# Kernel optimization log

Measured on AMD Instinct MI355X. Metric: run time of the kernel, lower is better.

## Reference

```python
import jax, jax.numpy as jnp
import numpy as np

INPUT_DIM = 1024
OUTPUT_DIM = 1024
DOWN = INPUT_DIM // 8  # reduction_factor=8
NUM_TOKENS = 2


def setup_inputs() -> dict:
    key = jax.random.key(0)
    k1, k2, k3, k4, k5 = jax.random.split(key, 5)
    B, Sx, Sy = 32, 2048, 512
    x = jax.random.normal(k1, (B, Sx, INPUT_DIM), dtype=jnp.float32)
    y = jax.random.normal(k2, (B, Sy, INPUT_DIM), dtype=jnp.float32)
    # nn.Parameter(torch.rand(...)) -> uniform [0,1)
    latent_tokens = jax.random.uniform(k3, (NUM_TOKENS, INPUT_DIM), dtype=jnp.float32)
    gate = jnp.zeros((1,), dtype=jnp.float32)
    # Conv1d kernel_size=1, no bias == pointwise matmul; kaiming-uniform-ish init
    lim_d = 1.0 / np.sqrt(INPUT_DIM)
    lim_u = 1.0 / np.sqrt(DOWN)
    W_down = jax.random.uniform(k4, (DOWN, INPUT_DIM), dtype=jnp.float32, minval=-lim_d, maxval=lim_d)
    W_up = jax.random.uniform(k5, (OUTPUT_DIM, DOWN), dtype=jnp.float32, minval=-lim_u, maxval=lim_u)
    return {"x": x, "y": y, "latent_tokens": latent_tokens, "gate": gate,
            "W_down": W_down, "W_up": W_up}


def reference(x, y, latent_tokens, gate, W_down, W_up):
    # tokens attend over y:  [B,T,Sy] softmax over Sy
    att_y2t = jax.nn.softmax(jnp.einsum('td,bsd->bts', latent_tokens, y), axis=-1)
    tokens = latent_tokens[None] + jnp.einsum('bts,bsd->btd', att_y2t, y)  # [B,T,D]
    # x attends over tokens: [B,Sx,T] softmax over T
    att_t2x = jax.nn.softmax(jnp.einsum('bsd,btd->bst', x, tokens), axis=-1)
    x_res = jnp.einsum('bst,btd->bsd', att_t2x, tokens)
    x = x + gate * x_res
    # 1x1 conv bottleneck: down -> ReLU -> up (pointwise matmuls)
    z = jax.nn.relu(jnp.einsum('bsd,ed->bse', x, W_down))
    out = jnp.einsum('bse,oe->bso', z, W_up)
    return out
```

## Files before the change

### kernel.cpp

```cpp
#include <hip/hip_runtime.h>
#include <hip/hip_bf16.h>

#define B_N 32
#define SX 2048
#define SY 512
#define DIM 1024
#define NTOK 2
#define DN 128
#define ODIM 1024
#define BM 64
#define QK 256
#define NQ 4

typedef __bf16 bf16;
typedef __bf16 bf16x8 __attribute__((ext_vector_type(8)));
typedef __bf16 bf16x4 __attribute__((ext_vector_type(4)));
typedef float f32x4 __attribute__((ext_vector_type(4)));

__device__ __forceinline__ f32x4 mfma16(bf16x8 a, bf16x8 b, f32x4 c) {
  return __builtin_amdgcn_mfma_f32_16x16x32_bf16(a, b, c, 0, 0, 0);
}

__global__ __launch_bounds__(256) void prep_kernel(const float* __restrict__ Wd,
                                                   const float* __restrict__ Wu,
                                                   bf16* __restrict__ wdb,
                                                   bf16* __restrict__ wub) {
  int i = blockIdx.x * 256 + threadIdx.x;
  if (i < DN * DIM) {
    wdb[i] = (bf16)Wd[i];
    wub[i] = (bf16)Wu[i];
  }
}

__global__ __launch_bounds__(256) void tokens_kernel(const float* __restrict__ y,
                                                     const float* __restrict__ lat,
                                                     const float* __restrict__ gate,
                                                     float* __restrict__ tokens) {
  if (gate[0] == 0.0f) return;
  __shared__ float s_lat[NTOK][DIM];
  __shared__ float s_sc[NTOK][SY];
  int b = blockIdx.x;
  int tid = threadIdx.x, wave = tid >> 6, lane = tid & 63;
  const float* yb = y + (size_t)b * SY * DIM;
  for (int i = tid; i < NTOK * DIM; i += 256) ((float*)s_lat)[i] = lat[i];
  __syncthreads();
  for (int s = wave * 128; s < wave * 128 + 128; ++s) {
    const float* yr = yb + (size_t)s * DIM;
    float d0 = 0.f, d1 = 0.f;
#pragma unroll
    for (int i = 0; i < 4; ++i) {
      f32x4 v = *(const f32x4*)(yr + lane * 4 + i * 256);
      f32x4 l0 = *(const f32x4*)(&s_lat[0][lane * 4 + i * 256]);
      f32x4 l1 = *(const f32x4*)(&s_lat[1][lane * 4 + i * 256]);
      d0 += v[0] * l0[0] + v[1] * l0[1] + v[2] * l0[2] + v[3] * l0[3];
      d1 += v[0] * l1[0] + v[1] * l1[1] + v[2] * l1[2] + v[3] * l1[3];
    }
#pragma unroll
    for (int off = 32; off > 0; off >>= 1) {
      d0 += __shfl_xor(d0, off);
      d1 += __shfl_xor(d1, off);
    }
    if (lane == 0) { s_sc[0][s] = d0; s_sc[1][s] = d1; }
  }
  __syncthreads();
  if (wave < 2) {
    float m = -3.4e38f;
    for (int s = lane; s < SY; s += 64) m = fmaxf(m, s_sc[wave][s]);
#pragma unroll
    for (int off = 32; off > 0; off >>= 1) m = fmaxf(m, __shfl_xor(m, off));
    float sum = 0.f;
    for (int s = lane; s < SY; s += 64) {
      float e = expf(s_sc[wave][s] - m);
      s_sc[wave][s] = e;
      sum += e;
    }
#pragma unroll
    for (int off = 32; off > 0; off >>= 1) sum += __shfl_xor(sum, off);
    float inv = 1.f / sum;
    for (int s = lane; s < SY; s += 64) s_sc[wave][s] *= inv;
  }
  __syncthreads();
  float a0[4] = {0.f, 0.f, 0.f, 0.f}, a1[4] = {0.f, 0.f, 0.f, 0.f};
  for (int s = 0; s < SY; ++s) {
    float p0 = s_sc[0][s], p1 = s_sc[1][s];
    const float* yr = yb + (size_t)s * DIM;
#pragma unroll
    for (int i = 0; i < 4; ++i) {
      float v = yr[tid + i * 256];
      a0[i] += p0 * v;
      a1[i] += p1 * v;
    }
  }
  float* tb = tokens + (size_t)b * NTOK * DIM;
#pragma unroll
  for (int i = 0; i < 4; ++i) {
    tb[tid + i * 256] = s_lat[0][tid + i * 256] + a0[i];
    tb[DIM + tid + i * 256] = s_lat[1][tid + i * 256] + a1[i];
  }
}

__global__ __launch_bounds__(256) void xprime_kernel(const float* __restrict__ x,
                                                     const float* __restrict__ gate,
                                                     const float* __restrict__ tokens,
                                                     float* __restrict__ xp) {
  float g = gate[0];
  if (g == 0.0f) return;
  __shared__ float s_tok[NTOK][DIM];
  __shared__ float s_c[BM][2];
  int tid = threadIdx.x, w = tid >> 6, lane = tid & 63;
  size_t m0 = (size_t)blockIdx.x * BM;
  int b = (int)(m0 / SX);
  const float* xb = x + m0 * DIM;
  const float* tokb = tokens + (size_t)b * NTOK * DIM;
  for (int i = tid; i < NTOK * DIM; i += 256) ((float*)s_tok)[i] = tokb[i];
  __syncthreads();
  for (int i = 0; i < 16; ++i) {
    int r = w * 16 + i;
    const float* xrow = xb + (size_t)r * DIM;
    float d0 = 0.f, d1 = 0.f;
#pragma unroll
    for (int c = 0; c < 4; ++c) {
      f32x4 v = *(const f32x4*)(xrow + lane * 4 + c * 256);
      f32x4 t0 = *(const f32x4*)(&s_tok[0][lane * 4 + c * 256]);
      f32x4 t1 = *(const f32x4*)(&s_tok[1][lane * 4 + c * 256]);
      d0 += v[0] * t0[0] + v[1] * t0[1] + v[2] * t0[2] + v[3] * t0[3];
      d1 += v[0] * t1[0] + v[1] * t1[1] + v[2] * t1[2] + v[3] * t1[3];
    }
#pragma unroll
    for (int off = 32; off > 0; off >>= 1) {
      d0 += __shfl_xor(d0, off);
      d1 += __shfl_xor(d1, off);
    }
    if (lane == 0) {
      float mm = fmaxf(d0, d1);
      float e0 = expf(d0 - mm), e1 = expf(d1 - mm);
      float inv = g / (e0 + e1);
      s_c[r][0] = e0 * inv;
      s_c[r][1] = e1 * inv;
    }
  }
  __syncthreads();
  float* xpb = xp + m0 * DIM;
  for (int r = w * 16; r < w * 16 + 16; ++r) {
    float c0 = s_c[r][0], c1 = s_c[r][1];
#pragma unroll
    for (int c = 0; c < 4; ++c) {
      f32x4 v = *(const f32x4*)(xb + (size_t)r * DIM + lane * 4 + c * 256);
      f32x4 t0 = *(const f32x4*)(&s_tok[0][lane * 4 + c * 256]);
      f32x4 t1 = *(const f32x4*)(&s_tok[1][lane * 4 + c * 256]);
      f32x4 o;
#pragma unroll
      for (int j = 0; j < 4; ++j) o[j] = v[j] + c0 * t0[j] + c1 * t1[j];
      *(f32x4*)(xpb + (size_t)r * DIM + lane * 4 + c * 256) = o;
    }
  }
}

__global__ __launch_bounds__(512, 4) void main_kernel(const float* __restrict__ x,
                                                      const float* __restrict__ gate,
                                                      const float* __restrict__ xp,
                                                      const bf16* __restrict__ wdb,
                                                      const bf16* __restrict__ wub,
                                                      float* __restrict__ out) {
  __shared__ bf16 xq[2][BM * QK];
  __shared__ bf16 zsm[BM * DN];

  int tid = threadIdx.x, w = tid >> 6, lane = tid & 63;
  int lq = lane >> 4, lr = lane & 15;
  size_t m0 = (size_t)blockIdx.x * BM;
  float g = gate[0];
  const float* xb = ((g != 0.f) ? xp : x) + m0 * DIM;

  int srow = tid >> 5;
  int scolb = (tid & 31) * 16;
  const float* xgp = xb + (size_t)srow * DIM + (tid & 31) * 8;

  f32x4 xs0[4], xs1[4];
  bf16x8 wdr[8];
  f32x4 acc[4] = {};

  const bf16* wdp = wdb + (size_t)(w * 16 + lr) * DIM + lq * 8;

  char* xls = (char*)xq;
  char* zls = (char*)zsm;

  auto XLOAD = [&](int q) {
#pragma unroll
    for (int i = 0; i < 4; ++i) {
      const float* p = xgp + (size_t)i * 16 * DIM + q * QK;
      xs0[i] = *(const f32x4*)p;
      xs1[i] = *(const f32x4*)(p + 4);
    }
  };
  auto WLOAD = [&](int q) {
#pragma unroll
    for (int kc = 0; kc < 8; ++kc)
      wdr[kc] = *(const bf16x8*)(wdp + q * QK + kc * 32);
  };
  auto XWRITE = [&](int buf) {
    char* base = xls + buf * (BM * QK * 2);
#pragma unroll
    for (int i = 0; i < 4; ++i) {
      int row = i * 16 + srow;
      bf16x8 o;
#pragma unroll
      for (int j = 0; j < 4; ++j) {
        o[j] = (bf16)xs0[i][j];
        o[4 + j] = (bf16)xs1[i][j];
      }
      *(bf16x8*)(base + row * (QK * 2) + (scolb ^ ((row & 7) << 4))) = o;
    }
  };
  auto COMP = [&](int buf) {
    const char* base = xls + buf * (BM * QK * 2);
#pragma unroll
    for (int kc = 0; kc < 8; ++kc) {
#pragma unroll
      for (int mt = 0; mt < 4; ++mt) {
        int row = mt * 16 + lr;
        bf16x8 xf = *(const bf16x8*)(base + row * (QK * 2) +
                                     ((kc * 64 + lq * 16) ^ ((row & 7) << 4)));
        acc[mt] = mfma16(wdr[kc], xf, acc[mt]);
      }
    }
  };

  XLOAD(0);
  WLOAD(0);
  XWRITE(0);
  __syncthreads();

#pragma unroll
  for (int q = 0; q < NQ; ++q) {
    if (q + 1 < NQ) XLOAD(q + 1);
    COMP(q & 1);
    if (q + 1 < NQ) WLOAD(q + 1);
    __syncthreads();
    if (q + 1 < NQ) XWRITE((q + 1) & 1);
    __syncthreads();
  }

#pragma unroll
  for (int mt = 0; mt < 4; ++mt) {
    int xr = mt * 16 + lr;
    int dn = w * 16 + lq * 4;
    bf16x4 pk;
#pragma unroll
    for (int r = 0; r < 4; ++r) pk[r] = (bf16)fmaxf(acc[mt][r], 0.f);
    *(bf16x4*)(zls + xr * (DN * 2) + ((dn * 2) ^ ((xr & 7) << 4))) = pk;
  }
  __syncthreads();

  bf16x8 zF[4][4];
#pragma unroll
  for (int mt = 0; mt < 4; ++mt)
#pragma unroll
    for (int kt = 0; kt < 4; ++kt) {
      int xr = mt * 16 + lr;
      zF[kt][mt] = *(const bf16x8*)(zls + xr * (DN * 2) +
                                    (((kt * 32 + lq * 8) * 2) ^ ((xr & 7) << 4)));
    }

  float* ob = out + m0 * ODIM;
#pragma unroll 2
  for (int oc16 = 0; oc16 < 8; ++oc16) {
    int base = w * 128 + oc16 * 16;
    bf16x8 wu[4];
#pragma unroll
    for (int kt = 0; kt < 4; ++kt)
      wu[kt] = *(const bf16x8*)(wub + (size_t)(base + lr) * DN + kt * 32 + lq * 8);
    f32x4 a2[4] = {};
#pragma unroll
    for (int kt = 0; kt < 4; ++kt)
#pragma unroll
      for (int mt = 0; mt < 4; ++mt)
        a2[mt] = mfma16(wu[kt], zF[kt][mt], a2[mt]);
#pragma unroll
    for (int mt = 0; mt < 4; ++mt)
      *(f32x4*)(ob + (size_t)(mt * 16 + lr) * ODIM + base + lq * 4) = a2[mt];
  }
}

extern "C" void kernel_launch(void* const* d_in, const int* in_sizes, int n_in,
                              void* d_out, int out_size, void* d_ws, size_t ws_size,
                              hipStream_t stream) {
  const float* x = (const float*)d_in[0];
  const float* y = (const float*)d_in[1];
  const float* lat = (const float*)d_in[2];
  const float* gate = (const float*)d_in[3];
  const float* Wd = (const float*)d_in[4];
  const float* Wu = (const float*)d_in[5];
  float* out = (float*)d_out;
  char* ws = (char*)d_ws;

  float* tokens = (float*)ws;
  bf16* wdb = (bf16*)(ws + 262144);
  bf16* wub = (bf16*)(ws + 524288);

  prep_kernel<<<(DN * DIM + 255) / 256, 256, 0, stream>>>(Wd, Wu, wdb, wub);
  tokens_kernel<<<B_N, 256, 0, stream>>>(y, lat, gate, tokens);
  xprime_kernel<<<(B_N * SX) / BM, 256, 0, stream>>>(x, gate, tokens, out);
  main_kernel<<<(B_N * SX) / BM, 512, 0, stream>>>(x, gate, out, wdb, wub, out);
}
```

Measured before the change: 159.7 us.

## Split fused down/up projection into two kernels with smaller K tile

```diff
diff --git a/kernel.cpp b/kernel.cpp
--- a/kernel.cpp
+++ b/kernel.cpp
@@ -9,8 +9,8 @@
 #define DN 128
 #define ODIM 1024
 #define BM 64
-#define QK 256
-#define NQ 4
+#define QK 128
+#define NQ 8
 
 typedef __bf16 bf16;
 typedef __bf16 bf16x8 __attribute__((ext_vector_type(8)));
@@ -156,14 +156,12 @@
   }
 }
 
-__global__ __launch_bounds__(512, 4) void main_kernel(const float* __restrict__ x,
-                                                      const float* __restrict__ gate,
-                                                      const float* __restrict__ xp,
-                                                      const bf16* __restrict__ wdb,
-                                                      const bf16* __restrict__ wub,
-                                                      float* __restrict__ out) {
+__global__ __launch_bounds__(512, 8) void phase1_kernel(const float* __restrict__ x,
+                                                        const float* __restrict__ gate,
+                                                        const float* __restrict__ xp,
+                                                        const bf16* __restrict__ wdb,
+                                                        float* __restrict__ outbuf) {
   __shared__ bf16 xq[2][BM * QK];
-  __shared__ bf16 zsm[BM * DN];
 
   int tid = threadIdx.x, w = tid >> 6, lane = tid & 63;
   int lq = lane >> 4, lr = lane & 15;
@@ -171,50 +169,43 @@
   float g = gate[0];
   const float* xb = ((g != 0.f) ? xp : x) + m0 * DIM;
 
-  int srow = tid >> 5;
-  int scolb = (tid & 31) * 16;
-  const float* xgp = xb + (size_t)srow * DIM + (tid & 31) * 8;
-
-  f32x4 xs0[4], xs1[4];
-  bf16x8 wdr[8];
+  int srow = tid >> 3;
+  int scolb = (tid & 7) * 32;
+  const float* xgp = xb + (size_t)srow * DIM + (tid & 7) * 16;
+
+  f32x4 xs[4];
+  bf16x8 wdr[4];
   f32x4 acc[4] = {};
 
   const bf16* wdp = wdb + (size_t)(w * 16 + lr) * DIM + lq * 8;
-
   char* xls = (char*)xq;
-  char* zls = (char*)zsm;
 
   auto XLOAD = [&](int q) {
 #pragma unroll
-    for (int i = 0; i < 4; ++i) {
-      const float* p = xgp + (size_t)i * 16 * DIM + q * QK;
-      xs0[i] = *(const f32x4*)p;
-      xs1[i] = *(const f32x4*)(p + 4);
-    }
+    for (int i = 0; i < 4; ++i) xs[i] = *(const f32x4*)(xgp + q * QK + i * 4);
   };
   auto WLOAD = [&](int q) {
 #pragma unroll
-    for (int kc = 0; kc < 8; ++kc)
-      wdr[kc] = *(const bf16x8*)(wdp + q * QK + kc * 32);
+    for (int kc = 0; kc < 4; ++kc) wdr[kc] = *(const bf16x8*)(wdp + q * QK + kc * 32);
   };
   auto XWRITE = [&](int buf) {
     char* base = xls + buf * (BM * QK * 2);
-#pragma unroll
-    for (int i = 0; i < 4; ++i) {
-      int row = i * 16 + srow;
-      bf16x8 o;
-#pragma unroll
-      for (int j = 0; j < 4; ++j) {
-        o[j] = (bf16)xs0[i][j];
-        o[4 + j] = (bf16)xs1[i][j];
-      }
-      *(bf16x8*)(base + row * (QK * 2) + (scolb ^ ((row & 7) << 4))) = o;
-    }
+    bf16x8 o0, o1;
+#pragma unroll
+    for (int j = 0; j < 4; ++j) {
+      o0[j] = (bf16)xs[0][j];
+      o0[4 + j] = (bf16)xs[1][j];
+      o1[j] = (bf16)xs[2][j];
+      o1[4 + j] = (bf16)xs[3][j];
+    }
+    int sw = (srow & 7) << 4;
+    *(bf16x8*)(base + srow * (QK * 2) + (scolb ^ sw)) = o0;
+    *(bf16x8*)(base + srow * (QK * 2) + ((scolb + 16) ^ sw)) = o1;
   };
   auto COMP = [&](int buf) {
     const char* base = xls + buf * (BM * QK * 2);
 #pragma unroll
-    for (int kc = 0; kc < 8; ++kc) {
+    for (int kc = 0; kc < 4; ++kc) {
 #pragma unroll
       for (int mt = 0; mt < 4; ++mt) {
         int row = mt * 16 + lr;
@@ -240,26 +231,32 @@
     __syncthreads();
   }
 
+  bf16* zgb = (bf16*)((char*)outbuf + (size_t)blockIdx.x * (BM * ODIM * 4));
 #pragma unroll
   for (int mt = 0; mt < 4; ++mt) {
     int xr = mt * 16 + lr;
-    int dn = w * 16 + lq * 4;
     bf16x4 pk;
 #pragma unroll
     for (int r = 0; r < 4; ++r) pk[r] = (bf16)fmaxf(acc[mt][r], 0.f);
-    *(bf16x4*)(zls + xr * (DN * 2) + ((dn * 2) ^ ((xr & 7) << 4))) = pk;
-  }
-  __syncthreads();
+    *(bf16x4*)(zgb + xr * DN + w * 16 + lq * 4) = pk;
+  }
+}
+
+__global__ __launch_bounds__(512, 4) void phase2_kernel(const bf16* __restrict__ wub,
+                                                        float* __restrict__ out) {
+  int tid = threadIdx.x, w = tid >> 6, lane = tid & 63;
+  int lq = lane >> 4, lr = lane & 15;
+  size_t m0 = (size_t)blockIdx.x * BM;
+  const bf16* zgb = (const bf16*)((const char*)out + (size_t)blockIdx.x * (BM * ODIM * 4));
 
   bf16x8 zF[4][4];
 #pragma unroll
   for (int mt = 0; mt < 4; ++mt)
 #pragma unroll
-    for (int kt = 0; kt < 4; ++kt) {
-      int xr = mt * 16 + lr;
-      zF[kt][mt] = *(const bf16x8*)(zls + xr * (DN * 2) +
-                                    (((kt * 32 + lq * 8) * 2) ^ ((xr & 7) << 4)));
-    }
+    for (int kt = 0; kt < 4; ++kt)
+      zF[kt][mt] = *(const bf16x8*)(zgb + (size_t)(mt * 16 + lr) * DN + kt * 32 + lq * 8);
+
+  __syncthreads();
 
   float* ob = out + m0 * ODIM;
 #pragma unroll 2
@@ -300,5 +297,6 @@
   prep_kernel<<<(DN * DIM + 255) / 256, 256, 0, stream>>>(Wd, Wu, wdb, wub);
   tokens_kernel<<<B_N, 256, 0, stream>>>(y, lat, gate, tokens);
   xprime_kernel<<<(B_N * SX) / BM, 256, 0, stream>>>(x, gate, tokens, out);
-  main_kernel<<<(B_N * SX) / BM, 512, 0, stream>>>(x, gate, out, wdb, wub, out);
-}
+  phase1_kernel<<<(B_N * SX) / BM, 512, 0, stream>>>(x, gate, out, wdb, out);
+  phase2_kernel<<<(B_N * SX) / BM, 512, 0, stream>>>(wub, out);
+}
```

Measured after the change: 173.3 us. 1.09x slower.
